# Performance work log

Measured on AMD Instinct MI355X. Metric: run time of the kernel, lower is better.

## Reference

```python
import jax, jax.numpy as jnp
import numpy as np

H = 1024  # hid_dim


def setup_inputs() -> dict:
    key = jax.random.key(0)
    k1, k2, k3, k4 = jax.random.split(key, 4)
    B, S = 64, 2048
    dec_out = jax.random.normal(k1, (B, H), dtype=jnp.float32)
    enc_outs = jax.random.normal(k2, (S, B, H), dtype=jnp.float32)
    # GeneralScorer W_a: Linear(H, H, bias=False); torch Linear: y = x @ W.T
    W_a = jax.random.normal(k3, (H, H), dtype=jnp.float32) / np.sqrt(H)
    # linear_out: Linear(2H, H, bias=False) since scorer == 'general'
    W_out = jax.random.normal(k4, (H, 2 * H), dtype=jnp.float32) / np.sqrt(2 * H)
    return {"dec_out": dec_out, "enc_outs": enc_outs, "W_a": W_a, "W_out": W_out}


def reference(dec_out, enc_outs, W_a, W_out):
    # GeneralScorer: project query then dot with each encoder state
    q = dec_out @ W_a.T                               # [B, H]
    scores = jnp.einsum('sbh,bh->bs', enc_outs, q)    # [B, S]
    weights = jax.nn.softmax(scores, axis=1)          # [B, S]
    # context = weights @ enc_outs (per batch)
    context = jnp.einsum('bs,sbh->bh', weights, enc_outs)  # [B, H]
    context = jnp.tanh(jnp.concatenate([context, dec_out], axis=1) @ W_out.T)
    return (context, weights)
```

## Files before the change

kernel.cpp:

```cpp
#include <hip/hip_runtime.h>
#include <math.h>

#define BB 64
#define SS 2048
#define HH 1024
#define NCHUNK 16
#define CHUNK 128

#define Q_OFF    0
#define PCTX_OFF (BB * HH)
#define PML_OFF  (PCTX_OFF + BB * NCHUNK * HH)
#define CTXF_OFF (PML_OFF + BB * NCHUNK * 2)

__global__ __launch_bounds__(256) void gemm64(
    const float* __restrict__ A0, const float* __restrict__ A1,
    const float* __restrict__ W, float* __restrict__ out,
    int nchunks, int do_tanh)
{
    __shared__ float A_lds[64 * 256];
    __shared__ float W_lds[4 * 256];
    const int t  = threadIdx.x;
    const int it = blockIdx.x;
    const int b  = t & 63;
    const int il = t >> 6;
    const int K  = nchunks << 8;
    float acc = 0.f;

    for (int kc = 0; kc < nchunks; ++kc) {
        for (int idx = t; idx < 64 * 64; idx += 256) {
            const int row = idx >> 6;
            const int g   = idx & 63;
            const float* src = (kc < 4) ? (A0 + row * 1024 + kc * 256)
                                        : (A1 + row * 1024 + (kc - 4) * 256);
            float4 v = *(const float4*)(src + g * 4);
            ((float4*)A_lds)[row * 64 + (g ^ row)] = v;
        }
        for (int idx = t; idx < 1024; idx += 256) {
            const int r2 = idx >> 8;
            const int cc = idx & 255;
            W_lds[idx] = W[(size_t)(it * 4 + r2) * K + kc * 256 + cc];
        }
        __syncthreads();
        #pragma unroll 8
        for (int j4 = 0; j4 < 64; ++j4) {
            float4 a  = ((const float4*)A_lds)[b * 64 + (j4 ^ b)];
            float4 wv = ((const float4*)W_lds)[il * 64 + j4];
            acc += a.x * wv.x + a.y * wv.y + a.z * wv.z + a.w * wv.w;
        }
        __syncthreads();
    }
    if (do_tanh) acc = tanhf(acc);
    out[b * 1024 + it * 4 + il] = acc;
}

__global__ __launch_bounds__(256) void attn_partial(
    const float* __restrict__ enc, const float* __restrict__ q,
    float* __restrict__ part_ctx, float* __restrict__ part_ml,
    float* __restrict__ scores_raw)
{
    __shared__ float q_lds[HH];
    __shared__ float ctx_lds[4][HH];
    __shared__ float ml_lds[4][2];

    const int t = threadIdx.x;
    const int c = blockIdx.x;
    const int b = blockIdx.y;

    for (int i = t; i < HH / 4; i += 256)
        ((float4*)q_lds)[i] = ((const float4*)(q + b * HH))[i];
    __syncthreads();

    const int w    = t >> 6;
    const int lane = t & 63;
    float m = -INFINITY, lsum = 0.f;
    float ctx[16];
    #pragma unroll
    for (int e = 0; e < 16; ++e) ctx[e] = 0.f;

    const int RPW = CHUNK / 4;
    for (int r = 0; r < RPW; ++r) {
        const int s = c * CHUNK + w * RPW + r;
        const float* row = enc + ((size_t)s * BB + b) * HH;
        float4 v[4];
        float partial = 0.f;
        #pragma unroll
        for (int k = 0; k < 4; ++k) {
            v[k] = *(const float4*)(row + k * 256 + 4 * lane);
            float4 qv = *(const float4*)(q_lds + k * 256 + 4 * lane);
            partial += v[k].x * qv.x + v[k].y * qv.y + v[k].z * qv.z + v[k].w * qv.w;
        }
        #pragma unroll
        for (int off = 32; off; off >>= 1)
            partial += __shfl_xor(partial, off, 64);
        const float sc = partial;
        if (lane == 0) scores_raw[b * SS + s] = sc;

        if (sc > m) {
            const float scale = expf(m - sc);
            lsum *= scale;
            #pragma unroll
            for (int e = 0; e < 16; ++e) ctx[e] *= scale;
            m = sc;
        }
        const float p = expf(sc - m);
        lsum += p;
        #pragma unroll
        for (int k = 0; k < 4; ++k) {
            ctx[4 * k + 0] += p * v[k].x;
            ctx[4 * k + 1] += p * v[k].y;
            ctx[4 * k + 2] += p * v[k].z;
            ctx[4 * k + 3] += p * v[k].w;
        }
    }

    if (lane == 0) { ml_lds[w][0] = m; ml_lds[w][1] = lsum; }
    #pragma unroll
    for (int k = 0; k < 4; ++k)
        *(float4*)&ctx_lds[w][k * 256 + 4 * lane] =
            make_float4(ctx[4 * k + 0], ctx[4 * k + 1], ctx[4 * k + 2], ctx[4 * k + 3]);
    __syncthreads();

    const float m0 = ml_lds[0][0], m1 = ml_lds[1][0], m2 = ml_lds[2][0], m3 = ml_lds[3][0];
    const float mb = fmaxf(fmaxf(m0, m1), fmaxf(m2, m3));
    const float f0 = expf(m0 - mb), f1 = expf(m1 - mb), f2 = expf(m2 - mb), f3 = expf(m3 - mb);
    const float lb = f0 * ml_lds[0][1] + f1 * ml_lds[1][1] + f2 * ml_lds[2][1] + f3 * ml_lds[3][1];

    float4 a0 = ((const float4*)&ctx_lds[0][0])[t];
    float4 a1 = ((const float4*)&ctx_lds[1][0])[t];
    float4 a2 = ((const float4*)&ctx_lds[2][0])[t];
    float4 a3 = ((const float4*)&ctx_lds[3][0])[t];
    float4 o;
    o.x = f0 * a0.x + f1 * a1.x + f2 * a2.x + f3 * a3.x;
    o.y = f0 * a0.y + f1 * a1.y + f2 * a2.y + f3 * a3.y;
    o.z = f0 * a0.z + f1 * a1.z + f2 * a2.z + f3 * a3.z;
    o.w = f0 * a0.w + f1 * a1.w + f2 * a2.w + f3 * a3.w;
    ((float4*)(part_ctx + ((size_t)b * NCHUNK + c) * HH))[t] = o;
    if (t == 0) {
        part_ml[(b * NCHUNK + c) * 2 + 0] = mb;
        part_ml[(b * NCHUNK + c) * 2 + 1] = lb;
    }
}

__global__ __launch_bounds__(256) void attn_combine(
    const float* __restrict__ part_ctx, const float* __restrict__ part_ml,
    float* __restrict__ ctx_final, float* __restrict__ wts)
{
    const int b = blockIdx.x;
    const int t = threadIdx.x;
    __shared__ float mls[NCHUNK][2];
    for (int i = t; i < NCHUNK * 2; i += 256)
        ((float*)mls)[i] = part_ml[b * NCHUNK * 2 + i];
    __syncthreads();

    float M = -INFINITY;
    #pragma unroll
    for (int c2 = 0; c2 < NCHUNK; ++c2) M = fmaxf(M, mls[c2][0]);
    float f[NCHUNK];
    float L = 0.f;
    #pragma unroll
    for (int c2 = 0; c2 < NCHUNK; ++c2) {
        f[c2] = expf(mls[c2][0] - M);
        L += f[c2] * mls[c2][1];
    }
    const float inv = 1.0f / L;

    float4 acc = make_float4(0.f, 0.f, 0.f, 0.f);
    #pragma unroll
    for (int c2 = 0; c2 < NCHUNK; ++c2) {
        float4 v = ((const float4*)(part_ctx + ((size_t)b * NCHUNK + c2) * HH))[t];
        acc.x += f[c2] * v.x; acc.y += f[c2] * v.y;
        acc.z += f[c2] * v.z; acc.w += f[c2] * v.w;
    }
    acc.x *= inv; acc.y *= inv; acc.z *= inv; acc.w *= inv;
    ((float4*)(ctx_final + (size_t)b * HH))[t] = acc;

    for (int s = t; s < SS; s += 256)
        wts[b * SS + s] = expf(wts[b * SS + s] - M) * inv;
}

extern "C" void kernel_launch(void* const* d_in, const int* in_sizes, int n_in,
                              void* d_out, int out_size, void* d_ws, size_t ws_size,
                              hipStream_t stream)
{
    const float* dec   = (const float*)d_in[0];
    const float* enc   = (const float*)d_in[1];
    const float* W_a   = (const float*)d_in[2];
    const float* W_out = (const float*)d_in[3];
    float* out = (float*)d_out;
    float* ws  = (float*)d_ws;

    float* q         = ws + Q_OFF;
    float* part_ctx  = ws + PCTX_OFF;
    float* part_ml   = ws + PML_OFF;
    float* ctx_final = ws + CTXF_OFF;
    float* wts       = out + BB * HH;

    gemm64<<<256, 256, 0, stream>>>(dec, dec, W_a, q, 4, 0);
    attn_partial<<<dim3(NCHUNK, BB), 256, 0, stream>>>(enc, q, part_ctx, part_ml, wts);
    attn_combine<<<BB, 256, 0, stream>>>(part_ctx, part_ml, ctx_final, wts);
    gemm64<<<256, 256, 0, stream>>>(ctx_final, dec, W_out, out, 8, 1);
}
```

Baseline: 208.5 us.

## Double-buffer encoder tiles into LDS with async global_load_lds in attention kernel

The attention partial kernel now streams 16-row tiles of encoder states into a double-buffered LDS region using direct global-to-LDS loads. The next tile's loads are issued before the current tile is computed, and an explicit vmcnt wait keeps them in flight. Each wave processes 4 rows per step with a batched online-softmax update and batched shuffle reductions. The aim is to hide HBM latency on the dominant 512MB encoder read, at the cost of 128KB of LDS per block, which limits occupancy, and of relying on hand-written waitcnt ordering.

```diff
diff --git a/kernel.cpp b/kernel.cpp
--- a/kernel.cpp
+++ b/kernel.cpp
@@ -6,11 +6,21 @@
 #define HH 1024
 #define NCHUNK 16
 #define CHUNK 128
+#define TILE 16
+#define NT (CHUNK / TILE)
+
+typedef float f4 __attribute__((ext_vector_type(4)));
 
 #define Q_OFF    0
 #define PCTX_OFF (BB * HH)
 #define PML_OFF  (PCTX_OFF + BB * NCHUNK * HH)
 #define CTXF_OFF (PML_OFF + BB * NCHUNK * 2)
+
+__device__ __forceinline__ void gll16(const float* gsrc, float* ldst) {
+    __builtin_amdgcn_global_load_lds(
+        (const __attribute__((address_space(1))) void*)gsrc,
+        (__attribute__((address_space(3))) void*)ldst, 16, 0, 0);
+}
 
 __global__ __launch_bounds__(256) void gemm64(
     const float* __restrict__ A0, const float* __restrict__ A1,
@@ -53,88 +63,126 @@
     out[b * 1024 + it * 4 + il] = acc;
 }
 
-__global__ __launch_bounds__(256) void attn_partial(
+__global__ __launch_bounds__(256) void attn_tile(
     const float* __restrict__ enc, const float* __restrict__ q,
     float* __restrict__ part_ctx, float* __restrict__ part_ml,
     float* __restrict__ scores_raw)
 {
-    __shared__ float q_lds[HH];
-    __shared__ float ctx_lds[4][HH];
-    __shared__ float ml_lds[4][2];
-
-    const int t = threadIdx.x;
-    const int c = blockIdx.x;
-    const int b = blockIdx.y;
-
-    for (int i = t; i < HH / 4; i += 256)
-        ((float4*)q_lds)[i] = ((const float4*)(q + b * HH))[i];
-    __syncthreads();
-
+    __shared__ float smem[2 * TILE * HH];
+    const int t    = threadIdx.x;
+    const int c    = blockIdx.x;
+    const int b    = blockIdx.y;
     const int w    = t >> 6;
     const int lane = t & 63;
+
+    f4 qreg[4];
+    #pragma unroll
+    for (int k = 0; k < 4; ++k)
+        qreg[k] = *(const f4*)(q + (size_t)b * HH + k * 256 + 4 * lane);
+
+    const size_t RS = (size_t)BB * HH;
+    const float* enc_b = enc + (size_t)b * HH + 4 * lane;
+
+    {
+        const int s0 = c * CHUNK + w * 4;
+        #pragma unroll
+        for (int i = 0; i < 16; ++i) {
+            const int r = i >> 2, seg = i & 3;
+            gll16(enc_b + (size_t)(s0 + r) * RS + seg * 256,
+                  smem + (w * 4 + r) * HH + seg * 256);
+        }
+    }
+
     float m = -INFINITY, lsum = 0.f;
-    float ctx[16];
-    #pragma unroll
-    for (int e = 0; e < 16; ++e) ctx[e] = 0.f;
-
-    const int RPW = CHUNK / 4;
-    for (int r = 0; r < RPW; ++r) {
-        const int s = c * CHUNK + w * RPW + r;
-        const float* row = enc + ((size_t)s * BB + b) * HH;
-        float4 v[4];
-        float partial = 0.f;
-        #pragma unroll
-        for (int k = 0; k < 4; ++k) {
-            v[k] = *(const float4*)(row + k * 256 + 4 * lane);
-            float4 qv = *(const float4*)(q_lds + k * 256 + 4 * lane);
-            partial += v[k].x * qv.x + v[k].y * qv.y + v[k].z * qv.z + v[k].w * qv.w;
-        }
-        #pragma unroll
-        for (int off = 32; off; off >>= 1)
-            partial += __shfl_xor(partial, off, 64);
-        const float sc = partial;
-        if (lane == 0) scores_raw[b * SS + s] = sc;
-
-        if (sc > m) {
-            const float scale = expf(m - sc);
-            lsum *= scale;
+    f4 ctxv[4];
+    #pragma unroll
+    for (int k = 0; k < 4; ++k) ctxv[k] = (f4)0.f;
+
+    #pragma unroll 2
+    for (int tt = 0; tt < NT; ++tt) {
+        if (tt + 1 < NT) {
+            float* buf_n = smem + ((tt + 1) & 1) * TILE * HH;
+            const int s0 = c * CHUNK + (tt + 1) * TILE + w * 4;
             #pragma unroll
-            for (int e = 0; e < 16; ++e) ctx[e] *= scale;
-            m = sc;
-        }
-        const float p = expf(sc - m);
-        lsum += p;
-        #pragma unroll
-        for (int k = 0; k < 4; ++k) {
-            ctx[4 * k + 0] += p * v[k].x;
-            ctx[4 * k + 1] += p * v[k].y;
-            ctx[4 * k + 2] += p * v[k].z;
-            ctx[4 * k + 3] += p * v[k].w;
-        }
-    }
-
-    if (lane == 0) { ml_lds[w][0] = m; ml_lds[w][1] = lsum; }
+            for (int i = 0; i < 16; ++i) {
+                const int r = i >> 2, seg = i & 3;
+                gll16(enc_b + (size_t)(s0 + r) * RS + seg * 256,
+                      buf_n + (w * 4 + r) * HH + seg * 256);
+            }
+            asm volatile("s_waitcnt vmcnt(16)" ::: "memory");
+        } else {
+            asm volatile("s_waitcnt vmcnt(0)" ::: "memory");
+        }
+        __builtin_amdgcn_sched_barrier(0);
+
+        const float* buf = smem + (tt & 1) * TILE * HH;
+        f4 v[4][4];
+        #pragma unroll
+        for (int r = 0; r < 4; ++r)
+            #pragma unroll
+            for (int k = 0; k < 4; ++k)
+                v[r][k] = *(const f4*)(buf + (w * 4 + r) * HH + k * 256 + 4 * lane);
+
+        float d[4];
+        #pragma unroll
+        for (int r = 0; r < 4; ++r) {
+            f4 s = v[r][0] * qreg[0];
+            s += v[r][1] * qreg[1];
+            s += v[r][2] * qreg[2];
+            s += v[r][3] * qreg[3];
+            d[r] = s.x + s.y + s.z + s.w;
+        }
+        #pragma unroll
+        for (int off = 32; off; off >>= 1) {
+            #pragma unroll
+            for (int r = 0; r < 4; ++r)
+                d[r] += __shfl_xor(d[r], off, 64);
+        }
+
+        const int sbase = c * CHUNK + tt * TILE + w * 4;
+        float sv = d[0];
+        sv = (lane == 1) ? d[1] : sv;
+        sv = (lane == 2) ? d[2] : sv;
+        sv = (lane == 3) ? d[3] : sv;
+        if (lane < 4) scores_raw[b * SS + sbase + lane] = sv;
+
+        const float mx = fmaxf(fmaxf(d[0], d[1]), fmaxf(d[2], d[3]));
+        const float nm = fmaxf(m, mx);
+        const float sc = expf(m - nm);
+        float p[4];
+        #pragma unroll
+        for (int r = 0; r < 4; ++r) p[r] = expf(d[r] - nm);
+        lsum = lsum * sc + p[0] + p[1] + p[2] + p[3];
+        m = nm;
+        #pragma unroll
+        for (int k = 0; k < 4; ++k)
+            ctxv[k] = ctxv[k] * sc
+                    + p[0] * v[0][k] + p[1] * v[1][k]
+                    + p[2] * v[2][k] + p[3] * v[3][k];
+    }
+
+    __syncthreads();
+    float* ctx_m = smem;
+    float* ml_m  = smem + 4 * HH;
+    if (lane == 0) { ml_m[w * 2] = m; ml_m[w * 2 + 1] = lsum; }
     #pragma unroll
     for (int k = 0; k < 4; ++k)
-        *(float4*)&ctx_lds[w][k * 256 + 4 * lane] =
-            make_float4(ctx[4 * k + 0], ctx[4 * k + 1], ctx[4 * k + 2], ctx[4 * k + 3]);
+        *(f4*)(ctx_m + w * HH + k * 256 + 4 * lane) = ctxv[k];
     __syncthreads();
 
-    const float m0 = ml_lds[0][0], m1 = ml_lds[1][0], m2 = ml_lds[2][0], m3 = ml_lds[3][0];
+    const float m0 = ml_m[0], l0 = ml_m[1], m1 = ml_m[2], l1 = ml_m[3];
+    const float m2 = ml_m[4], l2 = ml_m[5], m3 = ml_m[6], l3 = ml_m[7];
     const float mb = fmaxf(fmaxf(m0, m1), fmaxf(m2, m3));
-    const float f0 = expf(m0 - mb), f1 = expf(m1 - mb), f2 = expf(m2 - mb), f3 = expf(m3 - mb);
-    const float lb = f0 * ml_lds[0][1] + f1 * ml_lds[1][1] + f2 * ml_lds[2][1] + f3 * ml_lds[3][1];
-
-    float4 a0 = ((const float4*)&ctx_lds[0][0])[t];
-    float4 a1 = ((const float4*)&ctx_lds[1][0])[t];
-    float4 a2 = ((const float4*)&ctx_lds[2][0])[t];
-    float4 a3 = ((const float4*)&ctx_lds[3][0])[t];
-    float4 o;
-    o.x = f0 * a0.x + f1 * a1.x + f2 * a2.x + f3 * a3.x;
-    o.y = f0 * a0.y + f1 * a1.y + f2 * a2.y + f3 * a3.y;
-    o.z = f0 * a0.z + f1 * a1.z + f2 * a2.z + f3 * a3.z;
-    o.w = f0 * a0.w + f1 * a1.w + f2 * a2.w + f3 * a3.w;
-    ((float4*)(part_ctx + ((size_t)b * NCHUNK + c) * HH))[t] = o;
+    const float f0 = expf(m0 - mb), f1 = expf(m1 - mb);
+    const float f2 = expf(m2 - mb), f3 = expf(m3 - mb);
+    const float lb = f0 * l0 + f1 * l1 + f2 * l2 + f3 * l3;
+
+    const f4 a0 = ((const f4*)(ctx_m + 0 * HH))[t];
+    const f4 a1 = ((const f4*)(ctx_m + 1 * HH))[t];
+    const f4 a2 = ((const f4*)(ctx_m + 2 * HH))[t];
+    const f4 a3 = ((const f4*)(ctx_m + 3 * HH))[t];
+    const f4 o = f0 * a0 + f1 * a1 + f2 * a2 + f3 * a3;
+    ((f4*)(part_ctx + ((size_t)b * NCHUNK + c) * HH))[t] = o;
     if (t == 0) {
         part_ml[(b * NCHUNK + c) * 2 + 0] = mb;
         part_ml[(b * NCHUNK + c) * 2 + 1] = lb;
@@ -196,7 +244,7 @@
     float* wts       = out + BB * HH;
 
     gemm64<<<256, 256, 0, stream>>>(dec, dec, W_a, q, 4, 0);
-    attn_partial<<<dim3(NCHUNK, BB), 256, 0, stream>>>(enc, q, part_ctx, part_ml, wts);
+    attn_tile<<<dim3(NCHUNK, BB), 256, 0, stream>>>(enc, q, part_ctx, part_ml, wts);
     attn_combine<<<BB, 256, 0, stream>>>(part_ctx, part_ml, ctx_final, wts);
     gemm64<<<256, 256, 0, stream>>>(ctx_final, dec, W_out, out, 8, 1);
 }
```

After: 201.9 us, median of 2. 3.1% less time.

## Split attention into per-wave sequence slices with register prefetch and wider combine

Applied to the files above, without the earlier changes.

Reworks the attention pass so each wave handles one batch row over a short 16-step sequence slice. Neighbouring waves read adjacent batch rows, and the next row is prefetched with nontemporal loads. This removes the in-block LDS reduction and aims to improve memory-level parallelism and coalescing over the large encoder tensor. In exchange, the number of partial context vectors grows eightfold, which adds substantial workspace traffic and a heavier combine kernel running on only 64 blocks.

```diff
diff --git a/kernel.cpp b/kernel.cpp
--- a/kernel.cpp
+++ b/kernel.cpp
@@ -4,13 +4,15 @@
 #define BB 64
 #define SS 2048
 #define HH 1024
-#define NCHUNK 16
-#define CHUNK 128
+#define NS 128
+#define SC 16
+
+typedef float f4 __attribute__((ext_vector_type(4)));
 
 #define Q_OFF    0
 #define PCTX_OFF (BB * HH)
-#define PML_OFF  (PCTX_OFF + BB * NCHUNK * HH)
-#define CTXF_OFF (PML_OFF + BB * NCHUNK * 2)
+#define PML_OFF  (PCTX_OFF + BB * NS * HH)
+#define CTXF_OFF (PML_OFF + BB * NS * 2)
 
 __global__ __launch_bounds__(256) void gemm64(
     const float* __restrict__ A0, const float* __restrict__ A1,
@@ -53,91 +55,78 @@
     out[b * 1024 + it * 4 + il] = acc;
 }
 
-__global__ __launch_bounds__(256) void attn_partial(
+__global__ __launch_bounds__(512) void attn_row(
     const float* __restrict__ enc, const float* __restrict__ q,
     float* __restrict__ part_ctx, float* __restrict__ part_ml,
     float* __restrict__ scores_raw)
 {
-    __shared__ float q_lds[HH];
-    __shared__ float ctx_lds[4][HH];
-    __shared__ float ml_lds[4][2];
-
-    const int t = threadIdx.x;
-    const int c = blockIdx.x;
-    const int b = blockIdx.y;
-
-    for (int i = t; i < HH / 4; i += 256)
-        ((float4*)q_lds)[i] = ((const float4*)(q + b * HH))[i];
-    __syncthreads();
-
+    const int t    = threadIdx.x;
     const int w    = t >> 6;
     const int lane = t & 63;
+    const int bg   = blockIdx.x;
+    const int n    = blockIdx.y;
+    const int b    = bg * 8 + w;
+    const int s0   = n * SC;
+
+    f4 qreg[4];
+    #pragma unroll
+    for (int k = 0; k < 4; ++k)
+        qreg[k] = *(const f4*)(q + (size_t)b * HH + k * 256 + 4 * lane);
+
+    const size_t RS = (size_t)BB * HH;
+    const float* rp = enc + ((size_t)s0 * BB + b) * HH + 4 * lane;
+
+    f4 cur[4], nxt[4];
+    #pragma unroll
+    for (int k = 0; k < 4; ++k)
+        cur[k] = __builtin_nontemporal_load((const f4*)(rp + k * 256));
+
     float m = -INFINITY, lsum = 0.f;
-    float ctx[16];
+    f4 ctxv[4];
     #pragma unroll
-    for (int e = 0; e < 16; ++e) ctx[e] = 0.f;
+    for (int k = 0; k < 4; ++k) ctxv[k] = (f4)0.f;
 
-    const int RPW = CHUNK / 4;
-    for (int r = 0; r < RPW; ++r) {
-        const int s = c * CHUNK + w * RPW + r;
-        const float* row = enc + ((size_t)s * BB + b) * HH;
-        float4 v[4];
-        float partial = 0.f;
-        #pragma unroll
-        for (int k = 0; k < 4; ++k) {
-            v[k] = *(const float4*)(row + k * 256 + 4 * lane);
-            float4 qv = *(const float4*)(q_lds + k * 256 + 4 * lane);
-            partial += v[k].x * qv.x + v[k].y * qv.y + v[k].z * qv.z + v[k].w * qv.w;
+    for (int i = 0; i < SC; ++i) {
+        if (i + 1 < SC) {
+            const float* np = rp + RS;
+            #pragma unroll
+            for (int k = 0; k < 4; ++k)
+                nxt[k] = __builtin_nontemporal_load((const f4*)(np + k * 256));
         }
+        f4 sv = cur[0] * qreg[0];
+        sv += cur[1] * qreg[1];
+        sv += cur[2] * qreg[2];
+        sv += cur[3] * qreg[3];
+        float d = sv.x + sv.y + sv.z + sv.w;
         #pragma unroll
         for (int off = 32; off; off >>= 1)
-            partial += __shfl_xor(partial, off, 64);
-        const float sc = partial;
-        if (lane == 0) scores_raw[b * SS + s] = sc;
+            d += __shfl_xor(d, off, 64);
 
-        if (sc > m) {
-            const float scale = expf(m - sc);
-            lsum *= scale;
+        if (lane == 0) scores_raw[b * SS + s0 + i] = d;
+
+        const float nm = fmaxf(m, d);
+        const float e  = expf(m - nm);
+        const float p  = expf(d - nm);
+        lsum = lsum * e + p;
+        m = nm;
+        #pragma unroll
+        for (int k = 0; k < 4; ++k)
+            ctxv[k] = ctxv[k] * e + p * cur[k];
+
+        if (i + 1 < SC) {
             #pragma unroll
-            for (int e = 0; e < 16; ++e) ctx[e] *= scale;
-            m = sc;
-        }
-        const float p = expf(sc - m);
-        lsum += p;
-        #pragma unroll
-        for (int k = 0; k < 4; ++k) {
-            ctx[4 * k + 0] += p * v[k].x;
-            ctx[4 * k + 1] += p * v[k].y;
-            ctx[4 * k + 2] += p * v[k].z;
-            ctx[4 * k + 3] += p * v[k].w;
+            for (int k = 0; k < 4; ++k) cur[k] = nxt[k];
+            rp += RS;
         }
     }
 
-    if (lane == 0) { ml_lds[w][0] = m; ml_lds[w][1] = lsum; }
+    float* pc = part_ctx + ((size_t)b * NS + n) * HH + 4 * lane;
     #pragma unroll
     for (int k = 0; k < 4; ++k)
-        *(float4*)&ctx_lds[w][k * 256 + 4 * lane] =
-            make_float4(ctx[4 * k + 0], ctx[4 * k + 1], ctx[4 * k + 2], ctx[4 * k + 3]);
-    __syncthreads();
-
-    const float m0 = ml_lds[0][0], m1 = ml_lds[1][0], m2 = ml_lds[2][0], m3 = ml_lds[3][0];
-    const float mb = fmaxf(fmaxf(m0, m1), fmaxf(m2, m3));
-    const float f0 = expf(m0 - mb), f1 = expf(m1 - mb), f2 = expf(m2 - mb), f3 = expf(m3 - mb);
-    const float lb = f0 * ml_lds[0][1] + f1 * ml_lds[1][1] + f2 * ml_lds[2][1] + f3 * ml_lds[3][1];
-
-    float4 a0 = ((const float4*)&ctx_lds[0][0])[t];
-    float4 a1 = ((const float4*)&ctx_lds[1][0])[t];
-    float4 a2 = ((const float4*)&ctx_lds[2][0])[t];
-    float4 a3 = ((const float4*)&ctx_lds[3][0])[t];
-    float4 o;
-    o.x = f0 * a0.x + f1 * a1.x + f2 * a2.x + f3 * a3.x;
-    o.y = f0 * a0.y + f1 * a1.y + f2 * a2.y + f3 * a3.y;
-    o.z = f0 * a0.z + f1 * a1.z + f2 * a2.z + f3 * a3.z;
-    o.w = f0 * a0.w + f1 * a1.w + f2 * a2.w + f3 * a3.w;
-    ((float4*)(part_ctx + ((size_t)b * NCHUNK + c) * HH))[t] = o;
-    if (t == 0) {
-        part_ml[(b * NCHUNK + c) * 2 + 0] = mb;
-        part_ml[(b * NCHUNK + c) * 2 + 1] = lb;
+        *(f4*)(pc + k * 256) = ctxv[k];
+    if (lane == 0) {
+        part_ml[(b * NS + n) * 2 + 0] = m;
+        part_ml[(b * NS + n) * 2 + 1] = lsum;
     }
 }
 
@@ -147,33 +136,31 @@
 {
     const int b = blockIdx.x;
     const int t = threadIdx.x;
-    __shared__ float mls[NCHUNK][2];
-    for (int i = t; i < NCHUNK * 2; i += 256)
-        ((float*)mls)[i] = part_ml[b * NCHUNK * 2 + i];
+    __shared__ float mls[NS * 2];
+    __shared__ float fs[NS];
+    if (t < NS * 2) mls[t] = part_ml[b * NS * 2 + t];
     __syncthreads();
 
     float M = -INFINITY;
-    #pragma unroll
-    for (int c2 = 0; c2 < NCHUNK; ++c2) M = fmaxf(M, mls[c2][0]);
-    float f[NCHUNK];
+    #pragma unroll 8
+    for (int c = 0; c < NS; ++c) M = fmaxf(M, mls[2 * c]);
+    if (t < NS) fs[t] = expf(mls[2 * t] - M);
+    __syncthreads();
+
     float L = 0.f;
-    #pragma unroll
-    for (int c2 = 0; c2 < NCHUNK; ++c2) {
-        f[c2] = expf(mls[c2][0] - M);
-        L += f[c2] * mls[c2][1];
-    }
+    #pragma unroll 8
+    for (int c = 0; c < NS; ++c) L += fs[c] * mls[2 * c + 1];
     const float inv = 1.0f / L;
 
-    float4 acc = make_float4(0.f, 0.f, 0.f, 0.f);
+    f4 acc = (f4)0.f;
+    #pragma unroll 4
+    for (int c = 0; c < NS; ++c) {
+        const f4 v = *(const f4*)(part_ctx + ((size_t)b * NS + c) * HH + 4 * t);
+        acc += fs[c] * v;
+    }
+    *(f4*)(ctx_final + (size_t)b * HH + 4 * t) = acc * inv;
+
     #pragma unroll
-    for (int c2 = 0; c2 < NCHUNK; ++c2) {
-        float4 v = ((const float4*)(part_ctx + ((size_t)b * NCHUNK + c2) * HH))[t];
-        acc.x += f[c2] * v.x; acc.y += f[c2] * v.y;
-        acc.z += f[c2] * v.z; acc.w += f[c2] * v.w;
-    }
-    acc.x *= inv; acc.y *= inv; acc.z *= inv; acc.w *= inv;
-    ((float4*)(ctx_final + (size_t)b * HH))[t] = acc;
-
     for (int s = t; s < SS; s += 256)
         wts[b * SS + s] = expf(wts[b * SS + s] - M) * inv;
 }
@@ -196,7 +183,7 @@
     float* wts       = out + BB * HH;
 
     gemm64<<<256, 256, 0, stream>>>(dec, dec, W_a, q, 4, 0);
-    attn_partial<<<dim3(NCHUNK, BB), 256, 0, stream>>>(enc, q, part_ctx, part_ml, wts);
+    attn_row<<<dim3(8, NS), 512, 0, stream>>>(enc, q, part_ctx, part_ml, wts);
     attn_combine<<<BB, 256, 0, stream>>>(part_ctx, part_ml, ctx_final, wts);
     gemm64<<<256, 256, 0, stream>>>(ctx_final, dec, W_out, out, 8, 1);
 }
```

New measurement: 210.7 us. No clear change (+1.1%).
